# Optimization experiments

Hardware: AMD Instinct MI355X
Metric: run time of the kernel (lower is better)

The kernel has to match this reference:

```python
import jax, jax.numpy as jnp
import numpy as np

H = 24          # num_heads
QKV = 3 * 3072  # qkv_features * 3
EPS = 1e-6


def apply_rope(q, k, pe):
    # q,k: [B,H,L,D]; pe: [1,1,L,D//2,2,2]
    def rot(t):
        t_ = t.reshape(*t.shape[:-1], -1, 1, 2)  # [B,H,L,D/2,1,2]
        out = pe[..., 0] * t_[..., 0] + pe[..., 1] * t_[..., 1]  # [B,H,L,D/2,2]
        return out.reshape(t.shape)
    return rot(q), rot(k)


def setup_inputs() -> dict:
    key = jax.random.key(0)
    ks = jax.random.split(key, 8)
    B, L, D, Dh = 1, 2048, 3072, 128
    s = lambda n: 1.0 / np.sqrt(n)
    return {
        "x": jax.random.normal(ks[0], (B, L, D), jnp.float32),
        "vec": jax.random.normal(ks[1], (B, D), jnp.float32),
        "pe": jax.random.normal(ks[2], (1, 1, L, Dh // 2, 2, 2), jnp.float32),
        "w_mod": jax.random.normal(ks[3], (D, 3 * D), jnp.float32) * s(D),
        "b_mod": jnp.zeros((3 * D,), jnp.float32),
        "w1": jax.random.normal(ks[4], (D, QKV + 4 * D), jnp.float32) * s(D),
        "b1": jnp.zeros((QKV + 4 * D,), jnp.float32),
        "w2": jax.random.normal(ks[5], (D + 4 * D, D), jnp.float32) * s(5 * D),
        "b2": jnp.zeros((D,), jnp.float32),
        "q_scale": jnp.ones((Dh,), jnp.float32),
        "k_scale": jnp.ones((Dh,), jnp.float32),
    }


def reference(x, vec, pe, w_mod, b_mod, w1, b1, w2, b2, q_scale, k_scale):
    B, L, D = x.shape
    # modulation: silu + linear -> shift, scale, gate each [B,1,D]
    m = jax.nn.silu(vec) @ w_mod + b_mod
    shift, scale, gate = [t[:, None, :] for t in jnp.split(m, 3, axis=-1)]
    # pre-norm (LayerNorm, no scale/bias) + modulate
    mu = jnp.mean(x, axis=-1, keepdims=True)
    var = jnp.mean((x - mu) ** 2, axis=-1, keepdims=True)
    xn = (x - mu) * jax.lax.rsqrt(var + EPS)
    x_mod = (1.0 + scale) * xn + shift
    # fused qkv + mlp projection
    h = x_mod @ w1 + b1
    qkv, mlp = h[..., :QKV], h[..., QKV:]
    qkv = qkv.reshape(B, L, 3, H, -1).transpose(2, 0, 3, 1, 4)  # [3,B,H,L,Dh]
    q, k, v = qkv[0], qkv[1], qkv[2]
    # QK RMSNorm
    rms = lambda t, g: t * jax.lax.rsqrt(jnp.mean(t * t, axis=-1, keepdims=True) + EPS) * g
    q, k = rms(q, q_scale), rms(k, k_scale)
    # RoPE
    q, k = apply_rope(q, k, pe)
    # attention
    Dh = q.shape[-1]
    logits = jnp.einsum("bhqd,bhkd->bhqk", q, k) * (Dh ** -0.5)
    attn = jnp.einsum("bhqk,bhkd->bhqd", jax.nn.softmax(logits, axis=-1), v)
    attn = attn.transpose(0, 2, 1, 3).reshape(B, L, H * Dh)
    # parallel gated MLP + output projection
    out = jnp.concatenate((attn, jax.nn.gelu(mlp)), axis=-1) @ w2 + b2
    return x + gate * out
```

## Files before the change

### kernel.cpp

```cpp
#include <hip/hip_runtime.h>

typedef __bf16 bf16;
typedef __bf16 bf16x8 __attribute__((ext_vector_type(8)));
typedef float f32x4 __attribute__((ext_vector_type(4)));
typedef float f32x16 __attribute__((ext_vector_type(16)));

#define L_SEQ   2048
#define D_MODEL 3072
#define N_HEADS 24
#define N1      21504
#define QKV_N   9216
#define CC      15360


__device__ __forceinline__ void async_cp16(const void* g, void* s) {
    __builtin_amdgcn_global_load_lds((const __attribute__((address_space(1))) void*)g,
                                     (__attribute__((address_space(3))) void*)s, 16, 0, 0);
}

__global__ __launch_bounds__(256) void mod_init_kernel(const float* __restrict__ b_mod, float* __restrict__ m) {
    int j = blockIdx.x * 256 + threadIdx.x;
    m[j] = b_mod[j];
}

__global__ __launch_bounds__(256) void mod_gemv_kernel(const float* __restrict__ vec,
                                                       const float* __restrict__ w_mod,
                                                       float* __restrict__ m) {
    int j  = blockIdx.x * 256 + threadIdx.x;
    int d0 = blockIdx.y * 256;
    __shared__ float sv[256];
    float x = vec[d0 + threadIdx.x];
    sv[threadIdx.x] = x / (1.f + __expf(-x));
    __syncthreads();
    float acc = 0.f;
    #pragma unroll 8
    for (int d = 0; d < 256; d++)
        acc += sv[d] * w_mod[(size_t)(d0 + d) * QKV_N + j];
    atomicAdd(&m[j], acc);
}

__global__ __launch_bounds__(256) void ln_kernel(const float* __restrict__ x,
                                                 const float* __restrict__ m,
                                                 bf16* __restrict__ x_mod) {
    int l = blockIdx.x, tid = threadIdx.x;
    const float4* xr = (const float4*)(x + (size_t)l * D_MODEL);
    float4 v[3];
    float s = 0.f, ss = 0.f;
    #pragma unroll
    for (int p = 0; p < 3; p++) {
        v[p] = xr[p * 256 + tid];
        s  += v[p].x + v[p].y + v[p].z + v[p].w;
        ss += v[p].x * v[p].x + v[p].y * v[p].y + v[p].z * v[p].z + v[p].w * v[p].w;
    }
    #pragma unroll
    for (int off = 32; off; off >>= 1) { s += __shfl_xor(s, off); ss += __shfl_xor(ss, off); }
    __shared__ float rs[4], rss[4];
    int wave = tid >> 6, lane = tid & 63;
    if (lane == 0) { rs[wave] = s; rss[wave] = ss; }
    __syncthreads();
    s  = rs[0] + rs[1] + rs[2] + rs[3];
    ss = rss[0] + rss[1] + rss[2] + rss[3];
    float mu   = s * (1.f / D_MODEL);
    float var  = ss * (1.f / D_MODEL) - mu * mu;
    float rstd = rsqrtf(var + 1e-6f);
    #pragma unroll
    for (int p = 0; p < 3; p++) {
        int c = (p * 256 + tid) * 4;
        const float* ve = (const float*)&v[p];
        union { bf16 b[4]; uint2 u; } pk;
        #pragma unroll
        for (int e = 0; e < 4; e++) {
            float xn = (ve[e] - mu) * rstd;
            pk.b[e] = (bf16)((1.f + m[D_MODEL + c + e]) * xn + m[c + e]);
        }
        *(uint2*)(x_mod + (size_t)l * D_MODEL + c) = pk.u;
    }
}

__global__ __launch_bounds__(256) void tconv_kernel(const float* __restrict__ in, bf16* __restrict__ out,
                                                    int R, int C) {
    __shared__ float T[64][65];
    int c0 = blockIdx.x * 64, r0 = blockIdx.y * 64;
    int tid = threadIdx.x;
    int col4 = (tid & 15) * 4, rr = tid >> 4;
    #pragma unroll
    for (int p = 0; p < 4; p++) {
        int r = rr + p * 16;
        float4 v = *(const float4*)(in + (size_t)(r0 + r) * C + c0 + col4);
        T[r][col4 + 0] = v.x; T[r][col4 + 1] = v.y; T[r][col4 + 2] = v.z; T[r][col4 + 3] = v.w;
    }
    __syncthreads();
    int c = tid >> 2, rq = (tid & 3) * 16;
    union { bf16 b[16]; uint4 u[2]; } pk;
    #pragma unroll
    for (int i = 0; i < 16; i++) pk.b[i] = (bf16)T[rq + i][c];
    uint4* op = (uint4*)(out + (size_t)(c0 + c) * R + r0 + rq);
    op[0] = pk.u[0]; op[1] = pk.u[1];
}

template <int EPI>
__global__ __launch_bounds__(256, 3) void gemm_kernel(
    const bf16* __restrict__ A, const bf16* __restrict__ Bt,
    const float* __restrict__ bias, int K, int ld,
    bf16* __restrict__ o_qkv, bf16* __restrict__ o_concat,
    float* __restrict__ p0, float* __restrict__ p1) {
    __shared__ bf16 As[128 * 64];
    __shared__ bf16 Bs[128 * 64];
    const int tid = threadIdx.x;
    const int wave = tid >> 6, lane = tid & 63;
    const int l32 = lane & 31, lh = lane >> 5;
    const int wm = (wave >> 1) * 64, wn = (wave & 1) * 64;
    const int m0 = blockIdx.y * 128, n0 = blockIdx.x * 128;
    const int koff = (EPI == 2) ? blockIdx.z * K : 0;

    const int srow_i  = lane >> 3;
    const int schunk  = (lane & 7) ^ srow_i;
    const bf16* Agl = A  + (size_t)(m0 + wave * 8 + srow_i) * ld + koff + schunk * 8;
    const bf16* Bgl = Bt + (size_t)(n0 + wave * 8 + srow_i) * ld + koff + schunk * 8;
    bf16* As_w = As + wave * 8 * 64;
    bf16* Bs_w = Bs + wave * 8 * 64;

    f32x16 acc[2][2];
    #pragma unroll
    for (int i = 0; i < 2; i++)
        #pragma unroll
        for (int j = 0; j < 2; j++)
            #pragma unroll
            for (int e = 0; e < 16; e++) acc[i][j][e] = 0.f;

    const int sw = l32 & 7;

    for (int k0 = 0; k0 < K; k0 += 64) {
        __syncthreads();
        #pragma unroll
        for (int i = 0; i < 4; i++) {
            async_cp16(Agl + k0 + (size_t)(i * 32) * ld, As_w + i * 32 * 64);
            async_cp16(Bgl + k0 + (size_t)(i * 32) * ld, Bs_w + i * 32 * 64);
        }
        __syncthreads();
        #pragma unroll
        for (int ks = 0; ks < 4; ks++) {
            const int pos = ((ks * 2 + lh) ^ sw) * 8;
            bf16x8 a0 = *(const bf16x8*)(As + (wm +      l32) * 64 + pos);
            bf16x8 a1 = *(const bf16x8*)(As + (wm + 32 + l32) * 64 + pos);
            bf16x8 b0 = *(const bf16x8*)(Bs + (wn +      l32) * 64 + pos);
            bf16x8 b1 = *(const bf16x8*)(Bs + (wn + 32 + l32) * 64 + pos);
            acc[0][0] = __builtin_amdgcn_mfma_f32_32x32x16_bf16(a0, b0, acc[0][0], 0, 0, 0);
            acc[0][1] = __builtin_amdgcn_mfma_f32_32x32x16_bf16(a0, b1, acc[0][1], 0, 0, 0);
            acc[1][0] = __builtin_amdgcn_mfma_f32_32x32x16_bf16(a1, b0, acc[1][0], 0, 0, 0);
            acc[1][1] = __builtin_amdgcn_mfma_f32_32x32x16_bf16(a1, b1, acc[1][1], 0, 0, 0);
        }
    }

    float* po = (EPI == 2) ? (blockIdx.z ? p1 : p0) : nullptr;
    #pragma unroll
    for (int mt = 0; mt < 2; mt++) {
        #pragma unroll
        for (int nt = 0; nt < 2; nt++) {
            int col = n0 + wn + nt * 32 + l32;
            int rbase = m0 + wm + mt * 32 + 4 * lh;
            float bv = (EPI == 1) ? bias[col] : 0.f;
            #pragma unroll
            for (int r = 0; r < 16; r++) {
                int rr = rbase + (r & 3) + 8 * (r >> 2);
                float v = acc[mt][nt][r] + bv;
                if (EPI == 1) {
                    if (col < QKV_N) {
                        o_qkv[(size_t)rr * QKV_N + col] = (bf16)v;
                    } else {
                        float g = 0.5f * v * (1.f + tanhf(0.7978845608028654f * (v + 0.044715f * v * v * v)));
                        o_concat[(size_t)rr * CC + (col - QKV_N + D_MODEL)] = (bf16)g;
                    }
                } else {
                    po[(size_t)rr * D_MODEL + col] = v;
                }
            }
        }
    }
}

__global__ __launch_bounds__(256) void res_kernel(const float* __restrict__ p0, const float* __restrict__ p1,
                                                  const float* __restrict__ x, const float* __restrict__ gate,
                                                  const float* __restrict__ b2, float* __restrict__ out) {
    int i = blockIdx.x * 256 + threadIdx.x;
    float4 a  = ((const float4*)p0)[i];
    float4 b  = ((const float4*)p1)[i];
    float4 xr = ((const float4*)x)[i];
    int col = (i * 4) % D_MODEL;
    float4 g  = *(const float4*)(gate + col);
    float4 bb = *(const float4*)(b2 + col);
    float4 o;
    o.x = xr.x + g.x * (a.x + b.x + bb.x);
    o.y = xr.y + g.y * (a.y + b.y + bb.y);
    o.z = xr.z + g.z * (a.z + b.z + bb.z);
    o.w = xr.w + g.w * (a.w + b.w + bb.w);
    ((float4*)out)[i] = o;
}

__global__ __launch_bounds__(256) void qkv_rope_kernel(const bf16* __restrict__ hqkv,
                                                       const float* __restrict__ pe,
                                                       const float* __restrict__ q_scale,
                                                       const float* __restrict__ k_scale,
                                                       bf16* __restrict__ q_r, bf16* __restrict__ k_r) {
    int wave = threadIdx.x >> 6, lane = threadIdx.x & 63;
    int idx = blockIdx.x * 4 + wave;
    int l = idx / N_HEADS, h = idx - l * N_HEADS;
    const bf16* qg = hqkv + (size_t)l * QKV_N + h * 128;
    const bf16* kg = qg + D_MODEL;
    float q0 = (float)qg[2 * lane], q1 = (float)qg[2 * lane + 1];
    float k0 = (float)kg[2 * lane], k1 = (float)kg[2 * lane + 1];
    float sq = q0 * q0 + q1 * q1, sk = k0 * k0 + k1 * k1;
    #pragma unroll
    for (int off = 32; off; off >>= 1) { sq += __shfl_xor(sq, off); sk += __shfl_xor(sk, off); }
    float rq = rsqrtf(sq * (1.f / 128.f) + 1e-6f);
    float rk = rsqrtf(sk * (1.f / 128.f) + 1e-6f);
    float s0 = q_scale[2 * lane], s1 = q_scale[2 * lane + 1];
    float z0 = k_scale[2 * lane], z1 = k_scale[2 * lane + 1];
    float4 p = ((const float4*)pe)[(size_t)l * 64 + lane];
    float tq0 = q0 * rq * s0, tq1 = q1 * rq * s1;
    float tk0 = k0 * rk * z0, tk1 = k1 * rk * z1;
    size_t ob = ((size_t)h * L_SEQ + l) * 128 + 2 * lane;
    q_r[ob]     = (bf16)(p.x * tq0 + p.y * tq1);
    q_r[ob + 1] = (bf16)(p.z * tq0 + p.w * tq1);
    k_r[ob]     = (bf16)(p.x * tk0 + p.y * tk1);
    k_r[ob + 1] = (bf16)(p.z * tk0 + p.w * tk1);
}

__global__ __launch_bounds__(256) void vtrans_kernel(const bf16* __restrict__ hqkv, bf16* __restrict__ v_t) {
    int dt = blockIdx.x * 64, lt = blockIdx.y * 64, h = blockIdx.z;
    __shared__ bf16 T[64][72];
    int tid = threadIdx.x;
    #pragma unroll
    for (int p = 0; p < 2; p++) {
        int idx = p * 256 + tid;
        int r = idx >> 3, c = idx & 7;
        uint4 v = *(const uint4*)(hqkv + (size_t)(lt + r) * QKV_N + 2 * D_MODEL + h * 128 + dt + c * 8);
        *(uint4*)(&T[r][c * 8]) = v;
    }
    __syncthreads();
    #pragma unroll
    for (int p = 0; p < 2; p++) {
        int idx = p * 256 + tid;
        int d = idx >> 3, c = idx & 7;
        union { bf16 b[8]; uint4 u; } pk;
        #pragma unroll
        for (int i = 0; i < 8; i++) pk.b[i] = T[c * 8 + i][d];
        *(uint4*)(v_t + ((size_t)h * 128 + dt + d) * L_SEQ + lt + c * 8) = pk.u;
    }
}

#define QK_LD 136
#define VP_LD 72
__global__ __launch_bounds__(256) void attn_kernel(const bf16* __restrict__ q_r, const bf16* __restrict__ k_r,
                                                   const bf16* __restrict__ v_t, bf16* __restrict__ concat) {
    const int h = blockIdx.y;
    const int q0 = blockIdx.x * 64;
    __shared__ bf16 Ks[64 * QK_LD];
    __shared__ bf16 Vs[128 * VP_LD];
    __shared__ bf16 Ps[64 * VP_LD];
    const int tid = threadIdx.x, wave = tid >> 6, lane = tid & 63;
    const int l16 = lane & 15, lq = lane >> 4;
    const bf16* Qg = q_r + ((size_t)h * L_SEQ + q0) * 128;
    const bf16* Kg = k_r + (size_t)h * L_SEQ * 128;
    const bf16* Vg = v_t + (size_t)h * 128 * L_SEQ;
    bf16x8 aq[4];
    #pragma unroll
    for (int kk = 0; kk < 4; kk++)
        aq[kk] = *(const bf16x8*)(Qg + (size_t)(wave * 16 + l16) * 128 + kk * 32 + lq * 8);
    f32x4 accO[8];
    #pragma unroll
    for (int i = 0; i < 8; i++) accO[i] = f32x4{0.f, 0.f, 0.f, 0.f};
    float mrow[4] = {-1e30f, -1e30f, -1e30f, -1e30f};
    float lrow[4] = {0.f, 0.f, 0.f, 0.f};
    const float sc = 0.08838834764831845f * 1.4426950408889634f;
    for (int kt = 0; kt < 32; kt++) {
        __syncthreads();
        const bf16* Kt = Kg + (size_t)kt * 64 * 128;
        const bf16* Vt = Vg + kt * 64;
        #pragma unroll
        for (int p = 0; p < 4; p++) {
            int idx = p * 256 + tid, r = idx >> 4, c = idx & 15;
            *(uint4*)(Ks + r * QK_LD + c * 8) = *(const uint4*)(Kt + (size_t)r * 128 + c * 8);
        }
        #pragma unroll
        for (int p = 0; p < 4; p++) {
            int idx = p * 256 + tid, r = idx >> 3, c = idx & 7;
            *(uint4*)(Vs + r * VP_LD + c * 8) = *(const uint4*)(Vt + (size_t)r * L_SEQ + c * 8);
        }
        __syncthreads();
        f32x4 accS[4];
        #pragma unroll
        for (int i = 0; i < 4; i++) accS[i] = f32x4{0.f, 0.f, 0.f, 0.f};
        #pragma unroll
        for (int kk = 0; kk < 4; kk++) {
            #pragma unroll
            for (int nt = 0; nt < 4; nt++) {
                bf16x8 b = *(const bf16x8*)(Ks + (nt * 16 + l16) * QK_LD + kk * 32 + lq * 8);
                accS[nt] = __builtin_amdgcn_mfma_f32_16x16x32_bf16(aq[kk], b, accS[nt], 0, 0, 0);
            }
        }
        float alpha[4];
        #pragma unroll
        for (int r = 0; r < 4; r++) {
            float x0 = accS[0][r] * sc, x1 = accS[1][r] * sc, x2 = accS[2][r] * sc, x3 = accS[3][r] * sc;
            float mx = fmaxf(fmaxf(x0, x1), fmaxf(x2, x3));
            #pragma unroll
            for (int off = 1; off < 16; off <<= 1) mx = fmaxf(mx, __shfl_xor(mx, off));
            float mnew = fmaxf(mrow[r], mx);
            alpha[r] = __builtin_amdgcn_exp2f(mrow[r] - mnew);
            float p0 = __builtin_amdgcn_exp2f(x0 - mnew), p1 = __builtin_amdgcn_exp2f(x1 - mnew);
            float p2 = __builtin_amdgcn_exp2f(x2 - mnew), p3 = __builtin_amdgcn_exp2f(x3 - mnew);
            float rsum = p0 + p1 + p2 + p3;
            #pragma unroll
            for (int off = 1; off < 16; off <<= 1) rsum += __shfl_xor(rsum, off);
            lrow[r] = lrow[r] * alpha[r] + rsum;
            mrow[r] = mnew;
            int prow = wave * 16 + lq * 4 + r;
            Ps[prow * VP_LD +  0 + l16] = (bf16)p0;
            Ps[prow * VP_LD + 16 + l16] = (bf16)p1;
            Ps[prow * VP_LD + 32 + l16] = (bf16)p2;
            Ps[prow * VP_LD + 48 + l16] = (bf16)p3;
        }
        #pragma unroll
        for (int i = 0; i < 8; i++) {
            accO[i][0] *= alpha[0]; accO[i][1] *= alpha[1];
            accO[i][2] *= alpha[2]; accO[i][3] *= alpha[3];
        }
        #pragma unroll
        for (int kk = 0; kk < 2; kk++) {
            bf16x8 a = *(const bf16x8*)(Ps + (wave * 16 + l16) * VP_LD + kk * 32 + lq * 8);
            #pragma unroll
            for (int nt = 0; nt < 8; nt++) {
                bf16x8 b = *(const bf16x8*)(Vs + (nt * 16 + l16) * VP_LD + kk * 32 + lq * 8);
                accO[nt] = __builtin_amdgcn_mfma_f32_16x16x32_bf16(a, b, accO[nt], 0, 0, 0);
            }
        }
    }
    float inv[4];
    #pragma unroll
    for (int r = 0; r < 4; r++) inv[r] = 1.f / lrow[r];
    #pragma unroll
    for (int nt = 0; nt < 8; nt++)
        #pragma unroll
        for (int r = 0; r < 4; r++) {
            int row = q0 + wave * 16 + lq * 4 + r;
            concat[(size_t)row * CC + h * 128 + nt * 16 + l16] = (bf16)(accO[nt][r] * inv[r]);
        }
}

extern "C" void kernel_launch(void* const* d_in, const int* in_sizes, int n_in,
                              void* d_out, int out_size, void* d_ws, size_t ws_size,
                              hipStream_t stream) {
    const float* x       = (const float*)d_in[0];
    const float* vec     = (const float*)d_in[1];
    const float* pe      = (const float*)d_in[2];
    const float* w_mod   = (const float*)d_in[3];
    const float* b_mod   = (const float*)d_in[4];
    const float* w1      = (const float*)d_in[5];
    const float* b1      = (const float*)d_in[6];
    const float* w2      = (const float*)d_in[7];
    const float* b2      = (const float*)d_in[8];
    const float* q_scale = (const float*)d_in[9];
    const float* k_scale = (const float*)d_in[10];
    float* out = (float*)d_out;

    char* ws = (char*)d_ws;
    float* m_buf  = (float*)(ws);
    bf16* x_mod   = (bf16*)(ws + 36864);
    bf16* w1t     = (bf16*)(ws + 12619776);
    bf16* hqkv    = (bf16*)(ws + 144740352);
    bf16* concat  = (bf16*)(ws + 182489088);
    bf16* q_r     = (bf16*)(ws + 245403648);
    bf16* k_r     = (bf16*)(ws + 257986560);
    bf16* v_t     = (bf16*)(ws + 270569472);
    float* p0     = (float*)(ws + 144740352);
    float* p1     = (float*)(ws + 245403648);

    mod_init_kernel<<<36, 256, 0, stream>>>(b_mod, m_buf);
    mod_gemv_kernel<<<dim3(36, 12), 256, 0, stream>>>(vec, w_mod, m_buf);
    ln_kernel<<<L_SEQ, 256, 0, stream>>>(x, m_buf, x_mod);
    tconv_kernel<<<dim3(N1 / 64, D_MODEL / 64), 256, 0, stream>>>(w1, w1t, D_MODEL, N1);
    gemm_kernel<1><<<dim3(N1 / 128, L_SEQ / 128, 1), 256, 0, stream>>>(
        x_mod, w1t, b1, D_MODEL, D_MODEL, hqkv, concat, nullptr, nullptr);
    qkv_rope_kernel<<<L_SEQ * N_HEADS / 4, 256, 0, stream>>>(hqkv, pe, q_scale, k_scale, q_r, k_r);
    vtrans_kernel<<<dim3(2, 32, N_HEADS), 256, 0, stream>>>(hqkv, v_t);
    attn_kernel<<<dim3(32, N_HEADS), 256, 0, stream>>>(q_r, k_r, v_t, concat);
    tconv_kernel<<<dim3(D_MODEL / 64, CC / 64), 256, 0, stream>>>(w2, w1t, CC, D_MODEL);
    gemm_kernel<2><<<dim3(D_MODEL / 128, L_SEQ / 128, 2), 256, 0, stream>>>(
        concat, w1t, nullptr, CC / 2, CC, nullptr, nullptr, p0, p1);
    res_kernel<<<L_SEQ * D_MODEL / 1024, 256, 0, stream>>>(p0, p1, x, m_buf + 2 * D_MODEL, b2, out);
}
```

Measured before the change: 1.321 ms.

## Rewrite GEMM as 256x256 double-buffered 8-wave pipeline with staged async loads

Replaces the 128x128, 4-wave, single-buffered GEMM with a 256x256 tile computed by 8 waves using 16x16x32 MFMAs. K-tiles are double-buffered in LDS, with half-tile async global-to-LDS loads interleaved between MFMA quadrants, plus setprio hints and a grid swizzle for L2 locality. The aim is to hide global load latency behind compute and raise arithmetic intensity per block. It uses much more LDS and registers per block, and the fixed swizzle assumes an 8-wide grid dimension, which limits occupancy and flexibility.

```diff
diff --git a/kernel.cpp b/kernel.cpp
--- a/kernel.cpp
+++ b/kernel.cpp
@@ -98,85 +98,155 @@
     op[0] = pk.u[0]; op[1] = pk.u[1];
 }
 
+#define TILESZ 16384
+#define BUFSZ  32768
+
 template <int EPI>
-__global__ __launch_bounds__(256, 3) void gemm_kernel(
+__global__ __launch_bounds__(512, 2) void gemm_kernel(
     const bf16* __restrict__ A, const bf16* __restrict__ Bt,
     const float* __restrict__ bias, int K, int ld,
     bf16* __restrict__ o_qkv, bf16* __restrict__ o_concat,
     float* __restrict__ p0, float* __restrict__ p1) {
-    __shared__ bf16 As[128 * 64];
-    __shared__ bf16 Bs[128 * 64];
-    const int tid = threadIdx.x;
+    __shared__ bf16 lds[2 * BUFSZ];
+
+    const int tid  = threadIdx.x;
     const int wave = tid >> 6, lane = tid & 63;
-    const int l32 = lane & 31, lh = lane >> 5;
-    const int wm = (wave >> 1) * 64, wn = (wave & 1) * 64;
-    const int m0 = blockIdx.y * 128, n0 = blockIdx.x * 128;
+    const int mgrp = wave >> 2, ngrp = wave & 3;
+    const int l15 = lane & 15, l4 = lane >> 4, l7 = lane & 7;
+
+    const int flat = blockIdx.y * 8 + blockIdx.x;
+    const int nwg  = gridDim.y * 8;
+    const int swz  = (flat & 7) * (nwg >> 3) + (flat >> 3);
+    const int m0 = (swz & 7) * 256;
+    const int n0 = (swz >> 3) * 256;
     const int koff = (EPI == 2) ? blockIdx.z * K : 0;
-
-    const int srow_i  = lane >> 3;
-    const int schunk  = (lane & 7) ^ srow_i;
-    const bf16* Agl = A  + (size_t)(m0 + wave * 8 + srow_i) * ld + koff + schunk * 8;
-    const bf16* Bgl = Bt + (size_t)(n0 + wave * 8 + srow_i) * ld + koff + schunk * 8;
-    bf16* As_w = As + wave * 8 * 64;
-    bf16* Bs_w = Bs + wave * 8 * 64;
-
-    f32x16 acc[2][2];
-    #pragma unroll
-    for (int i = 0; i < 2; i++)
-        #pragma unroll
-        for (int j = 0; j < 2; j++)
-            #pragma unroll
-            for (int e = 0; e < 16; e++) acc[i][j][e] = 0.f;
-
-    const int sw = l32 & 7;
-
-    for (int k0 = 0; k0 < K; k0 += 64) {
-        __syncthreads();
-        #pragma unroll
-        for (int i = 0; i < 4; i++) {
-            async_cp16(Agl + k0 + (size_t)(i * 32) * ld, As_w + i * 32 * 64);
-            async_cp16(Bgl + k0 + (size_t)(i * 32) * ld, Bs_w + i * 32 * 64);
-        }
-        __syncthreads();
-        #pragma unroll
-        for (int ks = 0; ks < 4; ks++) {
-            const int pos = ((ks * 2 + lh) ^ sw) * 8;
-            bf16x8 a0 = *(const bf16x8*)(As + (wm +      l32) * 64 + pos);
-            bf16x8 a1 = *(const bf16x8*)(As + (wm + 32 + l32) * 64 + pos);
-            bf16x8 b0 = *(const bf16x8*)(Bs + (wn +      l32) * 64 + pos);
-            bf16x8 b1 = *(const bf16x8*)(Bs + (wn + 32 + l32) * 64 + pos);
-            acc[0][0] = __builtin_amdgcn_mfma_f32_32x32x16_bf16(a0, b0, acc[0][0], 0, 0, 0);
-            acc[0][1] = __builtin_amdgcn_mfma_f32_32x32x16_bf16(a0, b1, acc[0][1], 0, 0, 0);
-            acc[1][0] = __builtin_amdgcn_mfma_f32_32x32x16_bf16(a1, b0, acc[1][0], 0, 0, 0);
-            acc[1][1] = __builtin_amdgcn_mfma_f32_32x32x16_bf16(a1, b1, acc[1][1], 0, 0, 0);
-        }
+    const int nt = K >> 6;
+
+    const int srow   = lane >> 3;
+    const int schunk = (lane & 7) ^ srow;
+    const bf16* Ag = A  + (size_t)(m0 + wave * 8 + srow) * ld + koff + schunk * 8;
+    const bf16* Bg = Bt + (size_t)(n0 + wave * 8 + srow) * ld + koff + schunk * 8;
+    const size_t ld64  = (size_t)ld * 64;
+    const size_t ld128 = (size_t)ld * 128;
+    const int lw = wave * 8 * 64;
+
+#define STAGE_A(hh, tt, bb) { \
+    const bf16* _g = Ag + (size_t)(hh) * ld128 + (size_t)(tt) * 64; \
+    bf16* _l = lds + (bb) * BUFSZ + (hh) * 8192 + lw; \
+    async_cp16(_g, _l); \
+    async_cp16(_g + ld64, _l + 4096); }
+#define STAGE_B(hh, tt, bb) { \
+    const bf16* _g = Bg + (size_t)(hh) * ld128 + (size_t)(tt) * 64; \
+    bf16* _l = lds + (bb) * BUFSZ + TILESZ + (hh) * 8192 + lw; \
+    async_cp16(_g, _l); \
+    async_cp16(_g + ld64, _l + 4096); }
+#define LDA_H(mh, bb) { \
+    const bf16* _p = lds + (bb) * BUFSZ + (mh) * 8192 + (mgrp * 64 + l15) * 64; \
+    _Pragma("unroll") for (int i = 0; i < 4; i++) \
+    _Pragma("unroll") for (int kk = 0; kk < 2; kk++) \
+        aA[i][kk] = *(const bf16x8*)(_p + i * 1024 + ((kk * 4 + l4) ^ l7) * 8); }
+#define LDB_H(nh, bb) { \
+    const bf16* _p = lds + (bb) * BUFSZ + TILESZ + (nh) * 8192 + (ngrp * 32 + l15) * 64; \
+    _Pragma("unroll") for (int j = 0; j < 2; j++) \
+    _Pragma("unroll") for (int kk = 0; kk < 2; kk++) \
+        bB[j][kk] = *(const bf16x8*)(_p + j * 1024 + ((kk * 4 + l4) ^ l7) * 8); }
+#define MFMA_Q(mh, nh) { \
+    __builtin_amdgcn_s_setprio(1); \
+    _Pragma("unroll") for (int i = 0; i < 4; i++) \
+    _Pragma("unroll") for (int j = 0; j < 2; j++) \
+    _Pragma("unroll") for (int kk = 0; kk < 2; kk++) \
+        acc[(mh) * 4 + i][(nh) * 2 + j] = __builtin_amdgcn_mfma_f32_16x16x32_bf16( \
+            aA[i][kk], bB[j][kk], acc[(mh) * 4 + i][(nh) * 2 + j], 0, 0, 0); \
+    __builtin_amdgcn_s_setprio(0); }
+#define BAR()   __builtin_amdgcn_s_barrier()
+#define LGKM0() asm volatile("s_waitcnt lgkmcnt(0)" ::: "memory")
+
+    f32x4 acc[8][4];
+    #pragma unroll
+    for (int i = 0; i < 8; i++)
+        #pragma unroll
+        for (int j = 0; j < 4; j++)
+            acc[i][j] = f32x4{0.f, 0.f, 0.f, 0.f};
+
+    bf16x8 aA[4][2], bB[2][2];
+
+    STAGE_A(0, 0, 0); STAGE_A(1, 0, 0); STAGE_B(0, 0, 0); STAGE_B(1, 0, 0);
+    if (nt > 1) {
+        STAGE_A(0, 1, 1); STAGE_B(1, 1, 1);
+        asm volatile("s_waitcnt vmcnt(4)" ::: "memory");
+    } else {
+        asm volatile("s_waitcnt vmcnt(0)" ::: "memory");
+    }
+    BAR();
+
+    for (int u = 0; u < nt; ++u) {
+        const int b = u & 1;
+        LDA_H(0, b); LDB_H(0, b);
+        if (u + 1 < nt) STAGE_B(0, u + 1, b ^ 1);
+        BAR(); LGKM0();
+        MFMA_Q(0, 0);
+        BAR();
+        LDB_H(1, b);
+        if (u + 1 < nt) STAGE_A(1, u + 1, b ^ 1);
+        BAR(); LGKM0();
+        MFMA_Q(0, 1);
+        BAR();
+        LDA_H(1, b);
+        if (u + 2 < nt) STAGE_A(0, u + 2, b);
+        BAR(); LGKM0();
+        MFMA_Q(1, 1);
+        BAR();
+        LDB_H(0, b);
+        if (u + 2 < nt) STAGE_B(1, u + 2, b);
+        if (u + 1 < nt) {
+            if (u + 2 < nt) asm volatile("s_waitcnt vmcnt(4)" ::: "memory");
+            else            asm volatile("s_waitcnt vmcnt(0)" ::: "memory");
+        }
+        BAR(); LGKM0();
+        MFMA_Q(1, 0);
+        BAR();
     }
 
     float* po = (EPI == 2) ? (blockIdx.z ? p1 : p0) : nullptr;
     #pragma unroll
-    for (int mt = 0; mt < 2; mt++) {
-        #pragma unroll
-        for (int nt = 0; nt < 2; nt++) {
-            int col = n0 + wn + nt * 32 + l32;
-            int rbase = m0 + wm + mt * 32 + 4 * lh;
-            float bv = (EPI == 1) ? bias[col] : 0.f;
-            #pragma unroll
-            for (int r = 0; r < 16; r++) {
-                int rr = rbase + (r & 3) + 8 * (r >> 2);
-                float v = acc[mt][nt][r] + bv;
-                if (EPI == 1) {
-                    if (col < QKV_N) {
-                        o_qkv[(size_t)rr * QKV_N + col] = (bf16)v;
-                    } else {
+    for (int mh = 0; mh < 2; mh++)
+    #pragma unroll
+    for (int i = 0; i < 4; i++) {
+        const int rbase = m0 + mh * 128 + mgrp * 64 + i * 16 + l4 * 4;
+        #pragma unroll
+        for (int nh = 0; nh < 2; nh++)
+        #pragma unroll
+        for (int j = 0; j < 2; j++) {
+            const int col = n0 + nh * 128 + ngrp * 32 + j * 16 + l15;
+            f32x4 v4 = acc[mh * 4 + i][nh * 2 + j];
+            if (EPI == 1) {
+                const float bv = bias[col];
+                if (col < QKV_N) {
+                    #pragma unroll
+                    for (int r = 0; r < 4; r++)
+                        o_qkv[(size_t)(rbase + r) * QKV_N + col] = (bf16)(v4[r] + bv);
+                } else {
+                    #pragma unroll
+                    for (int r = 0; r < 4; r++) {
+                        float v = v4[r] + bv;
                         float g = 0.5f * v * (1.f + tanhf(0.7978845608028654f * (v + 0.044715f * v * v * v)));
-                        o_concat[(size_t)rr * CC + (col - QKV_N + D_MODEL)] = (bf16)g;
+                        o_concat[(size_t)(rbase + r) * CC + (col - QKV_N + D_MODEL)] = (bf16)g;
                     }
-                } else {
-                    po[(size_t)rr * D_MODEL + col] = v;
                 }
+            } else {
+                #pragma unroll
+                for (int r = 0; r < 4; r++)
+                    po[(size_t)(rbase + r) * D_MODEL + col] = v4[r];
             }
         }
     }
+#undef STAGE_A
+#undef STAGE_B
+#undef LDA_H
+#undef LDB_H
+#undef MFMA_Q
+#undef BAR
+#undef LGKM0
 }
 
 __global__ __launch_bounds__(256) void res_kernel(const float* __restrict__ p0, const float* __restrict__ p1,
@@ -380,13 +450,13 @@
     mod_gemv_kernel<<<dim3(36, 12), 256, 0, stream>>>(vec, w_mod, m_buf);
     ln_kernel<<<L_SEQ, 256, 0, stream>>>(x, m_buf, x_mod);
     tconv_kernel<<<dim3(N1 / 64, D_MODEL / 64), 256, 0, stream>>>(w1, w1t, D_MODEL, N1);
-    gemm_kernel<1><<<dim3(N1 / 128, L_SEQ / 128, 1), 256, 0, stream>>>(
+    gemm_kernel<1><<<dim3(L_SEQ / 256, N1 / 256, 1), 512, 0, stream>>>(
         x_mod, w1t, b1, D_MODEL, D_MODEL, hqkv, concat, nullptr, nullptr);
     qkv_rope_kernel<<<L_SEQ * N_HEADS / 4, 256, 0, stream>>>(hqkv, pe, q_scale, k_scale, q_r, k_r);
     vtrans_kernel<<<dim3(2, 32, N_HEADS), 256, 0, stream>>>(hqkv, v_t);
     attn_kernel<<<dim3(32, N_HEADS), 256, 0, stream>>>(q_r, k_r, v_t, concat);
     tconv_kernel<<<dim3(D_MODEL / 64, CC / 64), 256, 0, stream>>>(w2, w1t, CC, D_MODEL);
-    gemm_kernel<2><<<dim3(D_MODEL / 128, L_SEQ / 128, 2), 256, 0, stream>>>(
+    gemm_kernel<2><<<dim3(L_SEQ / 256, D_MODEL / 256, 2), 512, 0, stream>>>(
         concat, w1t, nullptr, CC / 2, CC, nullptr, nullptr, p0, p1);
     res_kernel<<<L_SEQ * D_MODEL / 1024, 256, 0, stream>>>(p0, p1, x, m_buf + 2 * D_MODEL, b2, out);
 }
```

After: 1.308 ms. Within noise of the previous version (-0.9%).
